# Optimization experiments

Measured on AMD Instinct MI355X. Metric: run time of the kernel, lower is better.

Reference implementation:

```python
import jax, jax.numpy as jnp
import numpy as np
import math

S, B, E, H = 2048, 2, 1024, 16
HD = E // H
NEG_INF = -jnp.inf


def setup_inputs() -> dict:
    key = jax.random.key(0)
    ks = jax.random.split(key, 6)
    query = jax.random.normal(ks[0], (S, B, E), dtype=jnp.float32)
    relative_pos_bias = jax.random.normal(ks[1], (H, S, S), dtype=jnp.float32)
    # causal float mask: 0 where allowed, -inf where disallowed (code tests attn_mask == -inf)
    causal = jnp.tril(jnp.ones((S, S), dtype=bool))
    attn_mask = jnp.where(causal, 0.0, NEG_INF).astype(jnp.float32)
    key_padding_mask = jnp.zeros((B, S), dtype=bool)
    in_proj_weight = jax.random.normal(ks[2], (3 * E, E), dtype=jnp.float32) / math.sqrt(E)
    in_proj_bias = jax.random.normal(ks[3], (3 * E,), dtype=jnp.float32) * 0.01
    out_proj_weight = jax.random.normal(ks[4], (E, E), dtype=jnp.float32) / math.sqrt(E)
    out_proj_bias = jax.random.normal(ks[5], (E,), dtype=jnp.float32) * 0.01
    return {
        "query": query,
        "relative_pos_bias": relative_pos_bias,
        "attn_mask": attn_mask,
        "key_padding_mask": key_padding_mask,
        "in_proj_weight": in_proj_weight,
        "in_proj_bias": in_proj_bias,
        "out_proj_weight": out_proj_weight,
        "out_proj_bias": out_proj_bias,
    }


def _nan_to_zero(x):
    return jnp.where(jnp.isnan(x), jnp.zeros_like(x), x)


def reference(query, relative_pos_bias, attn_mask, key_padding_mask,
              in_proj_weight, in_proj_bias, out_proj_weight, out_proj_bias):
    s, b, e = query.shape
    h, hd = H, HD
    # fused QKV projection from query (self-attention, matches F.linear(q, in_proj_weight))
    qkv = query @ in_proj_weight.T + in_proj_bias          # (S, B, 3E)
    q, k, v = jnp.split(qkv, 3, axis=-1)                   # each (S, B, E)
    # (S, B, E) -> (B, H, S, hd); torch does view(S, B*H, hd).transpose(0,1)
    def to_heads(x):
        return x.reshape(s, b, h, hd).transpose(1, 2, 0, 3)  # (B, H, S, hd)
    q, k, v = to_heads(q), to_heads(k), to_heads(v)
    scores = jnp.einsum("bhsd,bhtd->bhst", q, k) / math.sqrt(hd)  # (B, H, S, S)
    bias = jnp.clip(relative_pos_bias, -5.0, 5.0)
    scores = scores + bias[None] * 0.05
    scores = jnp.clip(scores, -30.0, 30.0)
    # attn_mask: -inf entries get masked
    scores = jnp.where((attn_mask == NEG_INF)[None, None], NEG_INF, scores)
    # key padding mask: True -> masked
    scores = jnp.where(key_padding_mask[:, None, None, :], NEG_INF, scores)
    attn_weights = jax.nn.softmax(scores, axis=-1)         # stable (max-subtracted)
    out = jnp.einsum("bhst,bhtd->bshd", attn_weights, v)   # (B, S, H, hd)
    out = _nan_to_zero(out).reshape(b, s, e)
    out = jnp.clip(out, -10.0, 10.0)
    out = out @ out_proj_weight.T + out_proj_bias
    out = _nan_to_zero(out)
    return out.transpose(1, 0, 2)                          # (S, B, E), batch_first=False
```

## Files before the change

### kernel.cpp

```cpp
#include <hip/hip_runtime.h>
#include <cstdint>

#define SS 2048
#define BB 2
#define EE 1024
#define HH 16
#define DD 64

typedef _Float16 f16;
typedef __attribute__((ext_vector_type(8))) _Float16 f16x8;
typedef __attribute__((ext_vector_type(4))) _Float16 f16x4;
typedef __attribute__((ext_vector_type(4))) float f32x4;

__device__ __forceinline__ f32x4 mfma16(f16x8 a, f16x8 b, f32x4 c) {
  return __builtin_amdgcn_mfma_f32_16x16x32_f16(a, b, c, 0, 0, 0);
}

__device__ __forceinline__ void gload16(void* lds, const void* g) {
  __builtin_amdgcn_global_load_lds((const __attribute__((address_space(1))) void*)g,
                                   (__attribute__((address_space(3))) void*)lds, 16, 0, 0);
}

__global__ void k_convert(const float* __restrict__ x, const float* __restrict__ wi,
                          const float* __restrict__ wo,
                          f16* __restrict__ xb, f16* __restrict__ wib, f16* __restrict__ wob) {
  const int N0 = 1048576, N1 = 786432, N2 = 262144;
  const int total = N0 + N1 + N2;
  for (int i = blockIdx.x * blockDim.x + threadIdx.x; i < total; i += gridDim.x * blockDim.x) {
    const float4* src; f16* dst; int off;
    if (i < N0)            { src = (const float4*)x;  dst = xb;  off = i; }
    else if (i < N0 + N1)  { src = (const float4*)wi; dst = wib; off = i - N0; }
    else                   { src = (const float4*)wo; dst = wob; off = i - N0 - N1; }
    float4 v = src[off];
    f16x4 o;
    o[0] = (f16)v.x; o[1] = (f16)v.y; o[2] = (f16)v.z; o[3] = (f16)v.w;
    *(f16x4*)(dst + (int64_t)off * 4) = o;
  }
}

__global__ __launch_bounds__(256) void k_gemm_qkv(
    const f16* __restrict__ A, const f16* __restrict__ Bw, const float* __restrict__ bias,
    f16* __restrict__ qo, f16* __restrict__ ko, f16* __restrict__ vt) {
  __shared__ __align__(16) f16 As[128 * 32];
  __shared__ __align__(16) f16 Bs[128 * 32];
  __shared__ __align__(16) f16 Cs[128 * 136];
  const int tid = threadIdx.x;
  const int w = tid >> 6, lane = tid & 63, g = lane >> 4, l4 = lane & 15;
  const int bm = blockIdx.y * 128, bn = blockIdx.x * 128;
  const int wr = (w >> 1) * 64, wc = (w & 1) * 64;
  f32x4 acc[4][4] = {};

  const f16* asrc[2]; const f16* bsrc[2]; f16* adst[2]; f16* bdst[2];
#pragma unroll
  for (int r = 0; r < 2; ++r) {
    int c = r * 256 + tid, row = c >> 2, cc = c & 3;
    asrc[r] = A + (int64_t)(bm + row) * 1024 + cc * 8;
    bsrc[r] = Bw + (int64_t)(bn + row) * 1024 + cc * 8;
    adst[r] = As + (r * 256 + w * 64) * 8;
    bdst[r] = Bs + (r * 256 + w * 64) * 8;
  }

  for (int kt = 0; kt < 1024; kt += 32) {
#pragma unroll
    for (int r = 0; r < 2; ++r) {
      gload16(adst[r], asrc[r] + kt);
      gload16(bdst[r], bsrc[r] + kt);
    }
    __syncthreads();
    f16x8 af[4], bf[4];
#pragma unroll
    for (int i = 0; i < 4; ++i) af[i] = *(const f16x8*)(As + (wr + i * 16 + l4) * 32 + g * 8);
#pragma unroll
    for (int j = 0; j < 4; ++j) bf[j] = *(const f16x8*)(Bs + (wc + j * 16 + l4) * 32 + g * 8);
#pragma unroll
    for (int i = 0; i < 4; ++i)
#pragma unroll
      for (int j = 0; j < 4; ++j)
        acc[i][j] = mfma16(af[i], bf[j], acc[i][j]);
    __syncthreads();
  }

  const int part = bn >> 10;
  const int baseh = (bn & 1023) >> 6;
  const float scale = (part == 0) ? 0.125f : 1.0f;

#pragma unroll
  for (int j = 0; j < 4; ++j) {
    const float bv = bias[bn + wc + j * 16 + l4];
#pragma unroll
    for (int i = 0; i < 4; ++i)
#pragma unroll
      for (int r = 0; r < 4; ++r)
        Cs[(wr + i * 16 + g * 4 + r) * 136 + wc + j * 16 + l4] =
            (f16)((acc[i][j][r] + bv) * scale);
  }
  __syncthreads();

  if (part < 2) {
    f16* dst = (part == 0) ? qo : ko;
#pragma unroll
    for (int it = 0; it < 8; ++it) {
      const int item = it * 256 + tid;
      const int m = item >> 4, c = item & 15;
      const int hh = baseh + (c >> 3), d0 = (c & 7) * 8;
      f16x8 v = *(const f16x8*)(Cs + m * 136 + (c >> 3) * 64 + d0);
      const int s = (bm >> 1) + (m >> 1), bq = m & 1;
      *(f16x8*)(dst + (((int64_t)(bq * HH + hh)) * SS + s) * DD + d0) = v;
    }
  } else {
#pragma unroll
    for (int it = 0; it < 8; ++it) {
      const int item = it * 256 + tid;
      const int s0 = item & 7, bq = (item >> 3) & 1, col = item >> 4;
      const int hh = baseh + (col >> 6), d = col & 63;
      f16x8 v;
#pragma unroll
      for (int k = 0; k < 8; ++k) v[k] = Cs[((s0 * 8 + k) * 2 + bq) * 136 + col];
      *(f16x8*)(vt + (((int64_t)(bq * HH + hh)) * DD + d) * SS + (bm >> 1) + s0 * 8) = v;
    }
  }
}

__global__ __launch_bounds__(256) void k_gemm_out(
    const f16* __restrict__ A, const f16* __restrict__ Bw, const float* __restrict__ bias,
    float* __restrict__ fo) {
  __shared__ __align__(16) f16 As[64 * 32];
  __shared__ __align__(16) f16 Bs[128 * 32];
  const int tid = threadIdx.x;
  const int w = tid >> 6, lane = tid & 63, g = lane >> 4, l4 = lane & 15;
  const int bm = blockIdx.y * 64, bn = blockIdx.x * 128;
  const int wr = (w >> 1) * 32, wc = (w & 1) * 64;
  f32x4 acc[2][4] = {};

  const f16* asrc = A + (int64_t)(bm + (tid >> 2)) * 1024 + (tid & 3) * 8;
  f16* adst = As + (w * 64) * 8;
  const f16* bsrc[2]; f16* bdst[2];
#pragma unroll
  for (int r = 0; r < 2; ++r) {
    int c = r * 256 + tid, row = c >> 2, cc = c & 3;
    bsrc[r] = Bw + (int64_t)(bn + row) * 1024 + cc * 8;
    bdst[r] = Bs + (r * 256 + w * 64) * 8;
  }

  for (int kt = 0; kt < 1024; kt += 32) {
    gload16(adst, asrc + kt);
#pragma unroll
    for (int r = 0; r < 2; ++r) gload16(bdst[r], bsrc[r] + kt);
    __syncthreads();
    f16x8 af[2], bf[4];
#pragma unroll
    for (int i = 0; i < 2; ++i) af[i] = *(const f16x8*)(As + (wr + i * 16 + l4) * 32 + g * 8);
#pragma unroll
    for (int j = 0; j < 4; ++j) bf[j] = *(const f16x8*)(Bs + (wc + j * 16 + l4) * 32 + g * 8);
#pragma unroll
    for (int i = 0; i < 2; ++i)
#pragma unroll
      for (int j = 0; j < 4; ++j)
        acc[i][j] = mfma16(af[i], bf[j], acc[i][j]);
    __syncthreads();
  }

#pragma unroll
  for (int i = 0; i < 2; ++i)
#pragma unroll
    for (int j = 0; j < 4; ++j) {
      const int n = bn + wc + j * 16 + l4;
      const float bv = bias[n];
#pragma unroll
      for (int r = 0; r < 4; ++r) {
        const int m = bm + wr + i * 16 + g * 4 + r;
        fo[(int64_t)m * EE + n] = acc[i][j][r] + bv;
      }
    }
}

__global__ __launch_bounds__(256) void k_attn(
    const f16* __restrict__ Qg, const f16* __restrict__ Kg, const f16* __restrict__ Vtg,
    const float* __restrict__ rpb, f16* __restrict__ Og) {
  __shared__ __align__(16) f16 Kt[2][64 * 64];
  __shared__ __align__(16) f16 Vt[2][64 * 64];
  __shared__ __align__(16) f16 Pt[64 * 64];
  __shared__ float sc_lds[64];
  __shared__ float li_lds[64];
  const int b = blockIdx.x, p = blockIdx.y, h = blockIdx.z;
  const int tid = threadIdx.x, w = tid >> 6, lane = tid & 63, g = lane >> 4, l4 = lane & 15;
  const int bh = b * HH + h;
  const float* rpbb = rpb + (int64_t)h * SS * SS;

#define ATTN_ITER(KT_, BCUR, BNXT)                                                      \
  {                                                                                     \
    const int kt_ = (KT_);                                                              \
    const int cur_ = kt_ & 1;                                                           \
    const int ks_ = kt_ * 64;                                                           \
    const bool pf_ = (kt_ < qt);                                                        \
    if (pf_) {                                                                          \
      const int ksn_ = ks_ + 64;                                                        \
      _Pragma("unroll")                                                                 \
      for (int r_ = 0; r_ < 2; ++r_) {                                                  \
        const int c_ = r_ * 256 + tid, row_ = c_ >> 3, cc_ = c_ & 7;                    \
        const int sc_ = cc_ ^ (row_ & 7);                                               \
        gload16(&Kt[cur_ ^ 1][(r_ * 256 + w * 64) * 8],                                 \
                Kg + ((int64_t)bh * SS + ksn_ + row_) * DD + sc_ * 8);                  \
        gload16(&Vt[cur_ ^ 1][(r_ * 256 + w * 64) * 8],                                 \
                Vtg + ((int64_t)bh * DD + row_) * SS + ksn_ + sc_ * 8);                 \
      }                                                                                 \
      asm volatile("" ::: "memory");           \
      _Pragma("unroll")                                                                 \
      for (int rg_ = 0; rg_ < 4; ++rg_)                                                 \
        _Pragma("unroll")                                                               \
        for (int j_ = 0; j_ < 4; ++j_)                                                  \
          BNXT[rg_ * 4 + j_] =                                                          \
              rpbb[(int64_t)(qrow + g * 4 + rg_) * SS + ksn_ + j_ * 16 + l4];           \
    }                                                                                   \
    f32x4 sf_[4] = {};                                                                  \
    _Pragma("unroll")                                                                   \
    for (int ki_ = 0; ki_ < 2; ++ki_)                                                   \
      _Pragma("unroll")                                                                 \
      for (int j_ = 0; j_ < 4; ++j_) {                                                  \
        const int row_ = j_ * 16 + l4;                                                  \
        const int ch_ = (ki_ * 4 + g) ^ (row_ & 7);                                     \
        f16x8 bk_ = *(const f16x8*)(&Kt[cur_][row_ * 64 + ch_ * 8]);                    \
        sf_[j_] = mfma16(qf[ki_], bk_, sf_[j_]);                                        \
      }                                                                                 \
    _Pragma("unroll")                                                                   \
    for (int rg_ = 0; rg_ < 4; ++rg_) {                                                 \
      const int qg_ = qrow + g * 4 + rg_;                                               \
      float pv_[4]; float mx_ = -INFINITY;                                              \
      _Pragma("unroll")                                                                 \
      for (int j_ = 0; j_ < 4; ++j_) {                                                  \
        const int kc_ = ks_ + j_ * 16 + l4;                                             \
        float bs_ = fminf(fmaxf(BCUR[rg_ * 4 + j_], -5.f), 5.f);                        \
        float v_ = sf_[j_][rg_] + 0.05f * bs_;                                          \
        v_ = fminf(fmaxf(v_, -30.f), 30.f);                                             \
        v_ = (kc_ > qg_) ? -INFINITY : v_;                                              \
        pv_[j_] = v_; mx_ = fmaxf(mx_, v_);                                             \
      }                                                                                 \
      _Pragma("unroll")                                                                 \
      for (int d_ = 1; d_ < 16; d_ <<= 1) mx_ = fmaxf(mx_, __shfl_xor(mx_, d_));        \
      const float mnew_ = fmaxf(m_run[rg_], mx_);                                       \
      const float scl_ = exp2f((m_run[rg_] - mnew_) * 1.44269504f);                     \
      float rsum_ = 0.f;                                                                \
      _Pragma("unroll")                                                                 \
      for (int j_ = 0; j_ < 4; ++j_) {                                                  \
        const float e_ = exp2f((pv_[j_] - mnew_) * 1.44269504f);                        \
        pv_[j_] = e_; rsum_ += e_;                                                      \
      }                                                                                 \
      _Pragma("unroll")                                                                 \
      for (int d_ = 1; d_ < 16; d_ <<= 1) rsum_ += __shfl_xor(rsum_, d_);               \
      l_run[rg_] = l_run[rg_] * scl_ + rsum_;                                           \
      m_run[rg_] = mnew_;                                                               \
      const int prow_ = w * 16 + g * 4 + rg_;                                           \
      if (l4 == 0) sc_lds[prow_] = scl_;                                                \
      _Pragma("unroll")                                                                 \
      for (int j_ = 0; j_ < 4; ++j_) {                                                  \
        const int col_ = j_ * 16 + l4;                                                  \
        const int ch_ = (col_ >> 3) ^ (prow_ & 7);                                      \
        Pt[prow_ * 64 + ch_ * 8 + (col_ & 7)] = (f16)pv_[j_];                           \
      }                                                                                 \
    }                                                                                   \
                                \
    const float osc_ = sc_lds[w * 16 + l4];                                             \
    _Pragma("unroll")                                                                   \
    for (int dt_ = 0; dt_ < 4; ++dt_) {                                                 \
      oacc[dt_][0] *= osc_; oacc[dt_][1] *= osc_;                                       \
      oacc[dt_][2] *= osc_; oacc[dt_][3] *= osc_;                                       \
    }                                                                                   \
    _Pragma("unroll")                                                                   \
    for (int ki_ = 0; ki_ < 2; ++ki_) {                                                 \
      const int prow_ = w * 16 + l4;                                                    \
      const int pch_ = (ki_ * 4 + g) ^ (prow_ & 7);                                     \
      f16x8 pb_ = *(const f16x8*)(&Pt[prow_ * 64 + pch_ * 8]);                          \
      _Pragma("unroll")                                                                 \
      for (int dt_ = 0; dt_ < 4; ++dt_) {                                               \
        const int vrow_ = dt_ * 16 + l4;                                                \
        const int vch_ = (ki_ * 4 + g) ^ (vrow_ & 7);                                   \
        f16x8 av_ = *(const f16x8*)(&Vt[cur_][vrow_ * 64 + vch_ * 8]);                  \
        oacc[dt_] = mfma16(av_, pb_, oacc[dt_]);                                        \
      }                                                                                 \
    }                                                                                   \
    asm volatile("s_waitcnt vmcnt(16)" ::: "memory");     \
    __builtin_amdgcn_s_barrier();                                                       \
  }

  for (int half = 0; half < 2; ++half) {
    const int qt = half ? p : (31 - p);
    const int qs = qt * 64;
    const int qrow = qs + w * 16;

    f16x8 qf[2];
    {
      const f16* qb = Qg + ((int64_t)bh * SS + qrow + l4) * DD + g * 8;
      qf[0] = *(const f16x8*)qb;
      qf[1] = *(const f16x8*)(qb + 32);
    }

    float bA[16], bB[16];
#pragma unroll
    for (int r_ = 0; r_ < 2; ++r_) {
      const int c_ = r_ * 256 + tid, row_ = c_ >> 3, cc_ = c_ & 7;
      const int sc_ = cc_ ^ (row_ & 7);
      gload16(&Kt[0][(r_ * 256 + w * 64) * 8], Kg + ((int64_t)bh * SS + row_) * DD + sc_ * 8);
      gload16(&Vt[0][(r_ * 256 + w * 64) * 8], Vtg + ((int64_t)bh * DD + row_) * SS + sc_ * 8);
    }
    asm volatile("" ::: "memory");
#pragma unroll
    for (int rg_ = 0; rg_ < 4; ++rg_)
#pragma unroll
      for (int j_ = 0; j_ < 4; ++j_)
        bA[rg_ * 4 + j_] = rpbb[(int64_t)(qrow + g * 4 + rg_) * SS + j_ * 16 + l4];
    asm volatile("s_waitcnt vmcnt(16)" ::: "memory");
    __builtin_amdgcn_s_barrier();

    f32x4 oacc[4] = {};
    float m_run[4], l_run[4];
#pragma unroll
    for (int r = 0; r < 4; ++r) { m_run[r] = -INFINITY; l_run[r] = 0.f; }

    int kt = 0;
    while (kt + 2 <= qt + 1) {
      ATTN_ITER(kt, bA, bB)
      ATTN_ITER(kt + 1, bB, bA)
      kt += 2;
    }
    if (kt <= qt) ATTN_ITER(kt, bA, bB)

    if (l4 == 0) {
#pragma unroll
      for (int rg = 0; rg < 4; ++rg) li_lds[w * 16 + g * 4 + rg] = 1.f / l_run[rg];
    }
    const float linv = li_lds[w * 16 + l4];
#pragma unroll
    for (int dt = 0; dt < 4; ++dt) {
#pragma unroll
      for (int r = 0; r < 4; ++r) {
        int d = dt * 16 + g * 4 + r;
        int ql = w * 16 + l4;
        float o = oacc[dt][r] * linv;
        o = fminf(fmaxf(o, -10.f), 10.f);
        int ch = (d >> 3) ^ (ql & 7);
        Pt[ql * 64 + ch * 8 + (d & 7)] = (f16)o;
      }
    }
    __syncthreads();
#pragma unroll
    for (int r = 0; r < 2; ++r) {
      int c = r * 256 + tid, row = c >> 3, cc = c & 7;
      int sc = cc ^ (row & 7);
      f16x8 ov = *(const f16x8*)(&Pt[row * 64 + sc * 8]);
      *(f16x8*)(Og + (((int64_t)(qs + row)) * BB + b) * EE + h * DD + cc * 8) = ov;
    }
  }
#undef ATTN_ITER
}

extern "C" void kernel_launch(void* const* d_in, const int* in_sizes, int n_in,
                              void* d_out, int out_size, void* d_ws, size_t ws_size,
                              hipStream_t stream) {
  (void)in_sizes; (void)n_in; (void)out_size; (void)ws_size;
  const float* query = (const float*)d_in[0];
  const float* rpb   = (const float*)d_in[1];
  const float* w_in  = (const float*)d_in[4];
  const float* b_in  = (const float*)d_in[5];
  const float* w_out = (const float*)d_in[6];
  const float* b_out = (const float*)d_in[7];
  float* out = (float*)d_out;

  f16* Xb  = (f16*)d_ws;
  f16* Wib = Xb + 4194304;
  f16* Wob = Wib + 3145728;
  f16* Qb  = Wob + 1048576;
  f16* Kb  = Qb + 4194304;
  f16* Vtb = Kb + 4194304;
  f16* Ob  = Xb;

  k_convert<<<2048, 256, 0, stream>>>(query, w_in, w_out, Xb, Wib, Wob);
  k_gemm_qkv<<<dim3(24, 32), 256, 0, stream>>>(Xb, Wib, b_in, Qb, Kb, Vtb);
  k_attn<<<dim3(2, 16, 16), 256, 0, stream>>>(Qb, Kb, Vtb, rpb, Ob);
  k_gemm_out<<<dim3(8, 64), 256, 0, stream>>>(Ob, Wob, b_out, out);
}
```

Measured before the change: 493.1 us.

## Deepen GEMM K-tile to 64 with XOR-swizzled LDS and block swizzle

Both projection GEMMs now stage 64-wide K slices instead of 32, which halves the number of barrier pairs per tile. An XOR swizzle on the 16-byte LDS chunks avoids bank conflicts on the wider rows. The 1D grid is remapped with a per-XCD style block swizzle so that neighbouring tiles share L2. The QKV kernel aliases its epilogue staging buffer onto the operand tiles to keep LDS use within budget, with no overlap of loads and compute added.

Measured after the change: 496.2 us. No clear change (+0.6%).

```diff
diff --git a/kernel.cpp b/kernel.cpp
--- a/kernel.cpp
+++ b/kernel.cpp
@@ -41,42 +41,56 @@
 __global__ __launch_bounds__(256) void k_gemm_qkv(
     const f16* __restrict__ A, const f16* __restrict__ Bw, const float* __restrict__ bias,
     f16* __restrict__ qo, f16* __restrict__ ko, f16* __restrict__ vt) {
-  __shared__ __align__(16) f16 As[128 * 32];
-  __shared__ __align__(16) f16 Bs[128 * 32];
-  __shared__ __align__(16) f16 Cs[128 * 136];
+  __shared__ __align__(16) char smem[34816];
+  f16* As = (f16*)smem;
+  f16* Bs = (f16*)(smem + 16384);
+  f16* Cs = (f16*)smem;
   const int tid = threadIdx.x;
   const int w = tid >> 6, lane = tid & 63, g = lane >> 4, l4 = lane & 15;
-  const int bm = blockIdx.y * 128, bn = blockIdx.x * 128;
+  const int swz = (blockIdx.x & 7) * 96 + (blockIdx.x >> 3);
+  const int bm = (swz / 24) * 128, bn = (swz % 24) * 128;
   const int wr = (w >> 1) * 64, wc = (w & 1) * 64;
   f32x4 acc[4][4] = {};
 
-  const f16* asrc[2]; const f16* bsrc[2]; f16* adst[2]; f16* bdst[2];
-#pragma unroll
-  for (int r = 0; r < 2; ++r) {
-    int c = r * 256 + tid, row = c >> 2, cc = c & 3;
-    asrc[r] = A + (int64_t)(bm + row) * 1024 + cc * 8;
-    bsrc[r] = Bw + (int64_t)(bn + row) * 1024 + cc * 8;
+  const f16* asrc[4]; const f16* bsrc[4]; f16* adst[4]; f16* bdst[4];
+#pragma unroll
+  for (int r = 0; r < 4; ++r) {
+    int c = r * 256 + tid, row = c >> 3, cc = c & 7;
+    int scc = cc ^ (row & 7);
+    asrc[r] = A + (int64_t)(bm + row) * 1024 + scc * 8;
+    bsrc[r] = Bw + (int64_t)(bn + row) * 1024 + scc * 8;
     adst[r] = As + (r * 256 + w * 64) * 8;
     bdst[r] = Bs + (r * 256 + w * 64) * 8;
   }
 
-  for (int kt = 0; kt < 1024; kt += 32) {
-#pragma unroll
-    for (int r = 0; r < 2; ++r) {
+  for (int kt = 0; kt < 1024; kt += 64) {
+#pragma unroll
+    for (int r = 0; r < 4; ++r) {
       gload16(adst[r], asrc[r] + kt);
       gload16(bdst[r], bsrc[r] + kt);
     }
     __syncthreads();
-    f16x8 af[4], bf[4];
-#pragma unroll
-    for (int i = 0; i < 4; ++i) af[i] = *(const f16x8*)(As + (wr + i * 16 + l4) * 32 + g * 8);
-#pragma unroll
-    for (int j = 0; j < 4; ++j) bf[j] = *(const f16x8*)(Bs + (wc + j * 16 + l4) * 32 + g * 8);
-#pragma unroll
-    for (int i = 0; i < 4; ++i)
-#pragma unroll
-      for (int j = 0; j < 4; ++j)
-        acc[i][j] = mfma16(af[i], bf[j], acc[i][j]);
+#pragma unroll
+    for (int kk = 0; kk < 2; ++kk) {
+      f16x8 af[4], bf[4];
+#pragma unroll
+      for (int i = 0; i < 4; ++i) {
+        const int row = wr + i * 16 + l4;
+        const int ch = (kk * 4 + g) ^ (row & 7);
+        af[i] = *(const f16x8*)(As + row * 64 + ch * 8);
+      }
+#pragma unroll
+      for (int j = 0; j < 4; ++j) {
+        const int row = wc + j * 16 + l4;
+        const int ch = (kk * 4 + g) ^ (row & 7);
+        bf[j] = *(const f16x8*)(Bs + row * 64 + ch * 8);
+      }
+#pragma unroll
+      for (int i = 0; i < 4; ++i)
+#pragma unroll
+        for (int j = 0; j < 4; ++j)
+          acc[i][j] = mfma16(af[i], bf[j], acc[i][j]);
+    }
     __syncthreads();
   }
 
@@ -124,39 +138,59 @@
 __global__ __launch_bounds__(256) void k_gemm_out(
     const f16* __restrict__ A, const f16* __restrict__ Bw, const float* __restrict__ bias,
     float* __restrict__ fo) {
-  __shared__ __align__(16) f16 As[64 * 32];
-  __shared__ __align__(16) f16 Bs[128 * 32];
+  __shared__ __align__(16) f16 As[64 * 64];
+  __shared__ __align__(16) f16 Bs[128 * 64];
   const int tid = threadIdx.x;
   const int w = tid >> 6, lane = tid & 63, g = lane >> 4, l4 = lane & 15;
-  const int bm = blockIdx.y * 64, bn = blockIdx.x * 128;
+  const int swz = (blockIdx.x & 7) * 64 + (blockIdx.x >> 3);
+  const int bm = (swz / 8) * 64, bn = (swz % 8) * 128;
   const int wr = (w >> 1) * 32, wc = (w & 1) * 64;
   f32x4 acc[2][4] = {};
 
-  const f16* asrc = A + (int64_t)(bm + (tid >> 2)) * 1024 + (tid & 3) * 8;
-  f16* adst = As + (w * 64) * 8;
-  const f16* bsrc[2]; f16* bdst[2];
+  const f16* asrc[2]; f16* adst[2];
 #pragma unroll
   for (int r = 0; r < 2; ++r) {
-    int c = r * 256 + tid, row = c >> 2, cc = c & 3;
-    bsrc[r] = Bw + (int64_t)(bn + row) * 1024 + cc * 8;
+    int c = r * 256 + tid, row = c >> 3, cc = c & 7;
+    int scc = cc ^ (row & 7);
+    asrc[r] = A + (int64_t)(bm + row) * 1024 + scc * 8;
+    adst[r] = As + (r * 256 + w * 64) * 8;
+  }
+  const f16* bsrc[4]; f16* bdst[4];
+#pragma unroll
+  for (int r = 0; r < 4; ++r) {
+    int c = r * 256 + tid, row = c >> 3, cc = c & 7;
+    int scc = cc ^ (row & 7);
+    bsrc[r] = Bw + (int64_t)(bn + row) * 1024 + scc * 8;
     bdst[r] = Bs + (r * 256 + w * 64) * 8;
   }
 
-  for (int kt = 0; kt < 1024; kt += 32) {
-    gload16(adst, asrc + kt);
-#pragma unroll
-    for (int r = 0; r < 2; ++r) gload16(bdst[r], bsrc[r] + kt);
+  for (int kt = 0; kt < 1024; kt += 64) {
+#pragma unroll
+    for (int r = 0; r < 2; ++r) gload16(adst[r], asrc[r] + kt);
+#pragma unroll
+    for (int r = 0; r < 4; ++r) gload16(bdst[r], bsrc[r] + kt);
     __syncthreads();
-    f16x8 af[2], bf[4];
-#pragma unroll
-    for (int i = 0; i < 2; ++i) af[i] = *(const f16x8*)(As + (wr + i * 16 + l4) * 32 + g * 8);
-#pragma unroll
-    for (int j = 0; j < 4; ++j) bf[j] = *(const f16x8*)(Bs + (wc + j * 16 + l4) * 32 + g * 8);
-#pragma unroll
-    for (int i = 0; i < 2; ++i)
-#pragma unroll
-      for (int j = 0; j < 4; ++j)
-        acc[i][j] = mfma16(af[i], bf[j], acc[i][j]);
+#pragma unroll
+    for (int kk = 0; kk < 2; ++kk) {
+      f16x8 af[2], bf[4];
+#pragma unroll
+      for (int i = 0; i < 2; ++i) {
+        const int row = wr + i * 16 + l4;
+        const int ch = (kk * 4 + g) ^ (row & 7);
+        af[i] = *(const f16x8*)(As + row * 64 + ch * 8);
+      }
+#pragma unroll
+      for (int j = 0; j < 4; ++j) {
+        const int row = wc + j * 16 + l4;
+        const int ch = (kk * 4 + g) ^ (row & 7);
+        bf[j] = *(const f16x8*)(Bs + row * 64 + ch * 8);
+      }
+#pragma unroll
+      for (int i = 0; i < 2; ++i)
+#pragma unroll
+        for (int j = 0; j < 4; ++j)
+          acc[i][j] = mfma16(af[i], bf[j], acc[i][j]);
+    }
     __syncthreads();
   }
 
@@ -374,7 +408,7 @@
   f16* Ob  = Xb;
 
   k_convert<<<2048, 256, 0, stream>>>(query, w_in, w_out, Xb, Wib, Wob);
-  k_gemm_qkv<<<dim3(24, 32), 256, 0, stream>>>(Xb, Wib, b_in, Qb, Kb, Vtb);
+  k_gemm_qkv<<<768, 256, 0, stream>>>(Xb, Wib, b_in, Qb, Kb, Vtb);
   k_attn<<<dim3(2, 16, 16), 256, 0, stream>>>(Qb, Kb, Vtb, rpb, Ob);
-  k_gemm_out<<<dim3(8, 64), 256, 0, stream>>>(Ob, Wob, b_out, out);
-}
+  k_gemm_out<<<512, 256, 0, stream>>>(Ob, Wob, b_out, out);
+}
```
